# Optimization experiments

Hardware: AMD Instinct MI355X
Metric: run time of the kernel (lower is better)

## Reference

```python
import jax, jax.numpy as jnp
from jax import lax
import numpy as np

HEADS, SAMPLES = 4, 8
B, C, D, H, W = 1, 64, 16, 64, 64
HD = C // HEADS  # head_dim = 16
BN_EPS = 1e-5


def conv3d(x, w, b=None, pad=0):
    out = lax.conv_general_dilated(
        x, w, (1, 1, 1), [(pad, pad)] * 3,
        dimension_numbers=("NCDHW", "OIDHW", "NCDHW"))
    if b is not None:
        out = out + b[None, :, None, None, None]
    return out


def trilinear_sample(vol, grid):
    # vol: [Dv,Hv,Wv,Cc]; grid: [...,3] with torch grid_sample semantics:
    # grid[...,0] -> x (W axis), grid[...,1] -> y (H axis), grid[...,2] -> z (D axis)
    # align_corners=True, padding_mode='border'. Returns [..., Cc].
    Dv, Hv, Wv, _ = vol.shape
    ix = (grid[..., 0] + 1.0) * 0.5 * (Wv - 1)
    iy = (grid[..., 1] + 1.0) * 0.5 * (Hv - 1)
    iz = (grid[..., 2] + 1.0) * 0.5 * (Dv - 1)
    x0 = jnp.floor(ix); y0 = jnp.floor(iy); z0 = jnp.floor(iz)
    wx = (ix - x0)[..., None]; wy = (iy - y0)[..., None]; wz = (iz - z0)[..., None]
    x0i = jnp.clip(x0.astype(jnp.int32), 0, Wv - 1); x1i = jnp.clip(x0i + 1, 0, Wv - 1)
    y0i = jnp.clip(y0.astype(jnp.int32), 0, Hv - 1); y1i = jnp.clip(y0i + 1, 0, Hv - 1)
    z0i = jnp.clip(z0.astype(jnp.int32), 0, Dv - 1); z1i = jnp.clip(z0i + 1, 0, Dv - 1)
    g = lambda z, y, x: vol[z, y, x]
    out = (g(z0i, y0i, x0i) * (1 - wz) * (1 - wy) * (1 - wx)
           + g(z0i, y0i, x1i) * (1 - wz) * (1 - wy) * wx
           + g(z0i, y1i, x0i) * (1 - wz) * wy * (1 - wx)
           + g(z0i, y1i, x1i) * (1 - wz) * wy * wx
           + g(z1i, y0i, x0i) * wz * (1 - wy) * (1 - wx)
           + g(z1i, y0i, x1i) * wz * (1 - wy) * wx
           + g(z1i, y1i, x0i) * wz * wy * (1 - wx)
           + g(z1i, y1i, x1i) * wz * wy * wx)
    return out


def t_deform(feat_prev, feat_curr, p):
    b, c, d, h, w = feat_curr.shape
    kv = conv3d(feat_prev, p["kv_w"], p["kv_b"])          # [B,2C,D,H,W]
    q = conv3d(feat_curr, p["q_w"], p["q_b"])              # [B,C,D,H,W]
    # offset branch: conv3x3 -> GELU(exact) -> conv3x3(no bias) -> tanh
    o = conv3d(feat_curr, p["off1_w"], p["off1_b"], pad=1)
    o = jax.nn.gelu(o, approximate=False)
    o = jnp.tanh(conv3d(o, p["off2_w"], None, pad=1))      # [B,M*S*3,D,H,W]
    off = o.reshape(b, HEADS, SAMPLES, 3, d, h, w).transpose(0, 1, 4, 5, 6, 2, 3)  # [B,M,D,H,W,S,3]
    zz, yy, xx = jnp.meshgrid(jnp.linspace(-1, 1, d), jnp.linspace(-1, 1, h),
                              jnp.linspace(-1, 1, w), indexing="ij")
    base = jnp.stack((zz, yy, xx), axis=-1).astype(feat_curr.dtype)  # [D,H,W,3]
    scale = jnp.array([d, h, w], dtype=feat_curr.dtype)
    grid = base[None, None, :, :, :, None, :] + off / scale
    grid = jnp.clip(grid, -1.0, 1.0)
    grid = grid.transpose(0, 1, 5, 2, 3, 4, 6).reshape(b * HEADS, SAMPLES, d, h, w, 3)
    # channels-last per (batch,head) volume; avoids torch's explicit repeat over samples
    vols = kv.reshape(b, HEADS, 2 * HD, d, h, w).transpose(0, 1, 3, 4, 5, 2)
    vols = vols.reshape(b * HEADS, d, h, w, 2 * HD)
    sampled = jax.vmap(trilinear_sample)(vols, grid)        # [B*M,S,D,H,W,2*HD]
    sampled = sampled.reshape(b, HEADS, SAMPLES, d, h, w, 2 * HD)
    key, value = sampled[..., :HD], sampled[..., HD:]
    qh = q.reshape(b, HEADS, HD, d, h, w) * (HD ** -0.5)
    attn = jnp.einsum("bmcdhw,bmsdhwc->bmsdhw", qh, key)
    attn = jax.nn.softmax(attn, axis=2)
    fused = jnp.einsum("bmsdhw,bmsdhwc->bmcdhw", attn, value).reshape(b, c, d, h, w)
    out = conv3d(fused, p["out_w"], p["out_b"])
    # BatchNorm3d (eval: running stats) + ReLU
    inv = lax.rsqrt(p["bn_var"] + BN_EPS)
    out = (out - p["bn_mean"][None, :, None, None, None]) * (inv * p["bn_gamma"])[None, :, None, None, None] \
          + p["bn_beta"][None, :, None, None, None]
    return jax.nn.relu(out)


def setup_inputs() -> dict:
    key = jax.random.key(0)
    ks = jax.random.split(key, 16)
    r = lambda k, shp, s=0.05: (jax.random.normal(k, shp, dtype=jnp.float32) * s)
    return {
        "mid_feat": jax.random.normal(ks[0], (B, C, D, H, W), dtype=jnp.float32),
        "occ_feat": jax.random.normal(ks[1], (B, C, D, H, W), dtype=jnp.float32),
        "prev_feat": jax.random.normal(ks[2], (B, C, D, H, W), dtype=jnp.float32),
        "off1_w": r(ks[3], (C, C, 3, 3, 3)), "off1_b": r(ks[4], (C,)),
        "off2_w": r(ks[5], (HEADS * SAMPLES * 3, C, 3, 3, 3)),
        "kv_w": r(ks[6], (2 * C, C, 1, 1, 1)), "kv_b": r(ks[7], (2 * C,)),
        "q_w": r(ks[8], (C, C, 1, 1, 1)), "q_b": r(ks[9], (C,)),
        "out_w": r(ks[10], (C, C, 1, 1, 1)), "out_b": r(ks[11], (C,)),
        "bn_gamma": jnp.ones((C,), jnp.float32), "bn_beta": jnp.zeros((C,), jnp.float32),
        "bn_mean": jnp.zeros((C,), jnp.float32), "bn_var": jnp.ones((C,), jnp.float32),
    }


def reference(mid_feat, occ_feat, prev_feat, off1_w, off1_b, off2_w, kv_w, kv_b,
              q_w, q_b, out_w, out_b, bn_gamma, bn_beta, bn_mean, bn_var):
    p = dict(off1_w=off1_w, off1_b=off1_b, off2_w=off2_w, kv_w=kv_w, kv_b=kv_b,
             q_w=q_w, q_b=q_b, out_w=out_w, out_b=out_b, bn_gamma=bn_gamma,
             bn_beta=bn_beta, bn_mean=bn_mean, bn_var=bn_var)
    d1 = t_deform(mid_feat, occ_feat, p)
    d2 = t_deform(mid_feat, prev_feat, p)
    return jnp.concatenate([mid_feat, d1, d2], axis=1)  # [B,3C,D,H,W]
```

## Files before the change

### kernel.cpp

```cpp
#include <hip/hip_runtime.h>
#include <math.h>

#define DD 16
#define HH 64
#define WW 64
#define VV (DD*HH*WW)
#define CC 64
#define NHEADS 4
#define NSAMP 8
#define HDIM 16

typedef unsigned int uint;
typedef unsigned short ushort;
typedef __attribute__((ext_vector_type(8))) short bf16x8;
typedef __attribute__((ext_vector_type(4))) float f32x4;

__device__ __forceinline__ float clampf(float v, float lo, float hi){ return fminf(fmaxf(v, lo), hi); }
__device__ __forceinline__ int imin(int a, int b){ return a < b ? a : b; }

__device__ __forceinline__ ushort f2bf(float f){
  uint u = __float_as_uint(f);
  uint r = (u + 0x7fffu + ((u>>16)&1u)) >> 16;
  return (ushort)r;
}
__device__ __forceinline__ uint packbf2(float a, float b){
  return (uint)f2bf(a) | ((uint)f2bf(b) << 16);
}
__device__ __forceinline__ float bflo(uint u){ return __uint_as_float(u << 16); }
__device__ __forceinline__ float bfhi(uint u){ return __uint_as_float(u & 0xffff0000u); }
__device__ __forceinline__ float bf2f(ushort u){ return __uint_as_float((uint)u << 16); }

__device__ __forceinline__ float fast_tanh(float x){
  float e = __expf(2.f*x);
  return 1.f - 2.f/(e + 1.f);
}

__device__ __forceinline__ bf16x8 make_af(const float* __restrict__ w, int mt, int ks, int lane){
  const float* p = w + (size_t)(mt*16 + (lane&15))*CC + ks*32 + ((lane>>4)<<3);
  float4 f0 = *reinterpret_cast<const float4*>(p);
  float4 f1 = *reinterpret_cast<const float4*>(p+4);
  union { uint4 u; bf16x8 b; } r;
  r.u.x = packbf2(f0.x, f0.y); r.u.y = packbf2(f0.z, f0.w);
  r.u.z = packbf2(f1.x, f1.y); r.u.w = packbf2(f1.z, f1.w);
  return r.b;
}

__device__ __forceinline__ void repack_wmfma_body(const float* __restrict__ w,
                                                  uint* __restrict__ o, int MG, int U){
  int j2 = U & 3;
  int m  = (U>>2) & 15;
  int q  = (U>>6) & 3;
  int rest = U >> 8;
  int g = rest % MG;
  int s = rest / MG;
  int tap = s >> 1, h = s & 1;
  int co = g*16 + m;
  int ci = h*32 + q*8 + j2*2;
  int base = co*1728 + ci*27 + tap;
  o[U] = packbf2(w[base], w[base + 27]);
}
__device__ __forceinline__ void repack_w1_body(const float* __restrict__ w,
                                               uint* __restrict__ o, int MT, int U){
  int j2 = U & 3;
  int lane = (U>>2) & 63;
  int frag = U >> 8;
  int mt = frag % MT;
  int ks = frag / MT;
  int q = lane >> 4, m = lane & 15;
  int co = mt*16 + m;
  int ci = ks*32 + q*8 + j2*2;
  o[U] = packbf2(w[co*CC + ci], w[co*CC + ci + 1]);
}

template<int CO, int EPI>
__device__ void conv1_body(
    int bid, int tid,
    const float* __restrict__ xa, const float* __restrict__ xb,
    const float* __restrict__ wraw, const float* __restrict__ bias,
    void* __restrict__ outp, float* __restrict__ mcopy)
{
  constexpr int MT = CO/16;
  constexpr int MW = MT/4;
  __shared__ ushort xt[64*72];
  int lane = tid & 63;
  int g = __builtin_amdgcn_readfirstlane(tid >> 6);
  int q = lane >> 4, n = lane & 15;
  int call = bid >> 10;
  int v0 = (bid & 1023) * 64;
  bf16x8 afr[2][MW];
  #pragma unroll
  for (int ks=0; ks<2; ks++)
    #pragma unroll
    for (int mw=0; mw<MW; mw++)
      afr[ks][mw] = make_af(wraw, g*MW+mw, ks, lane);
  const float* x = call ? xb : xa;
  for (int it = tid; it < 64*32; it += 256){
    int vox = it & 63; int cp = it >> 6;
    float a = x[(size_t)(2*cp)*VV + v0 + vox];
    float b = x[(size_t)(2*cp+1)*VV + v0 + vox];
    if constexpr (EPI == 0){
      mcopy[(size_t)(2*cp)*VV + v0 + vox] = a;
      mcopy[(size_t)(2*cp+1)*VV + v0 + vox] = b;
    }
    *reinterpret_cast<uint*>(&xt[vox*72 + 2*cp]) = packbf2(a,b);
  }
  __syncthreads();
  f32x4 acc[MW][4];
  #pragma unroll
  for (int mw=0;mw<MW;mw++)
    #pragma unroll
    for (int nt=0;nt<4;nt++){ acc[mw][nt].x=0.f; acc[mw][nt].y=0.f; acc[mw][nt].z=0.f; acc[mw][nt].w=0.f; }
  const char* ldsb = reinterpret_cast<const char*>(xt);
  #pragma unroll
  for (int ks=0; ks<2; ks++){
    bf16x8 bfr[4];
    #pragma unroll
    for (int nt=0; nt<4; nt++)
      bfr[nt] = *reinterpret_cast<const bf16x8*>(ldsb + ((nt*16+n)*144 + q*16 + ks*64));
    #pragma unroll
    for (int mw=0; mw<MW; mw++)
      #pragma unroll
      for (int nt=0; nt<4; nt++)
        acc[mw][nt] = __builtin_amdgcn_mfma_f32_16x16x32_bf16(afr[ks][mw], bfr[nt], acc[mw][nt], 0, 0, 0);
  }
  if constexpr (EPI == 0){
    #pragma unroll
    for (int mw=0; mw<MW; mw++){
      int mt = g*MW + mw;
      int cob = mt*16 + q*4;
      #pragma unroll
      for (int nt=0; nt<4; nt++){
        int v = v0 + nt*16 + n;
        float r0 = acc[mw][nt].x + bias[cob+0];
        float r1 = acc[mw][nt].y + bias[cob+1];
        float r2 = acc[mw][nt].z + bias[cob+2];
        float r3 = acc[mw][nt].w + bias[cob+3];
        int z = v >> 12, y = (v >> 6) & 63, xx = v & 63;
        int head = cob >> 5;
        uint* vols = (uint*)outp;
        uint2 pk; pk.x = packbf2(r0,r1); pk.y = packbf2(r2,r3);
        *reinterpret_cast<uint2*>(vols + ((size_t)head*VV + (size_t)(y*WW+xx)*DD + z)*16 + ((cob&31)>>1)) = pk;
      }
    }
  } else {
    __syncthreads();
    ushort* xr = xt;
    int cob = g*16 + q*4;
    #pragma unroll
    for (int nt=0; nt<4; nt++){
      int vox = nt*16 + n;
      uint2 pk;
      pk.x = packbf2((acc[0][nt].x + bias[cob+0])*0.25f, (acc[0][nt].y + bias[cob+1])*0.25f);
      pk.y = packbf2((acc[0][nt].z + bias[cob+2])*0.25f, (acc[0][nt].w + bias[cob+3])*0.25f);
      *reinterpret_cast<uint2*>(&xr[vox*64 + cob]) = pk;
    }
    __syncthreads();
    char* ob = (char*)((ushort*)outp + (size_t)call*CC*VV) + (size_t)v0*128;
    const char* lb = reinterpret_cast<const char*>(xr);
    #pragma unroll
    for (int k=0; k<2; k++){
      int idx = tid + k*256;
      *reinterpret_cast<uint4*>(ob + idx*16) = *reinterpret_cast<const uint4*>(lb + idx*16);
    }
  }
}

__global__ __launch_bounds__(256) void fused_front(
    const float* __restrict__ occ, const float* __restrict__ prev,
    const float* __restrict__ mid, uint* __restrict__ o0pk,
    const float* __restrict__ off1w, uint* __restrict__ wA1,
    const float* __restrict__ off2w, uint* __restrict__ wA2,
    const float* __restrict__ outw,  uint* __restrict__ wo,
    const float* __restrict__ kvw,  const float* __restrict__ kvb,
    const float* __restrict__ qw,   const float* __restrict__ qb,
    void* __restrict__ vols, void* __restrict__ qbuf, float* __restrict__ out)
{
  int b = blockIdx.x, tid = threadIdx.x;
  if (b < 1024){
    int idx = b*256 + tid;
    int v4 = (idx & (VV/4 - 1)) * 4;
    int rest = idx >> 14;
    int cg = rest & 7;
    int call = rest >> 3;
    const float* x = call ? prev : occ;
    const float* p0 = x + (size_t)(cg*8)*VV + v4;
    float4 f[8];
    #pragma unroll
    for (int c=0;c<8;c++) f[c] = *reinterpret_cast<const float4*>(p0 + (size_t)c*VV);
    uint4* ob = reinterpret_cast<uint4*>(o0pk) + (size_t)(call*8 + cg)*VV + v4;
    #pragma unroll
    for (int j=0;j<4;j++){
      float* fp = reinterpret_cast<float*>(f);
      uint4 w;
      w.x = packbf2(fp[0*4+j], fp[1*4+j]);
      w.y = packbf2(fp[2*4+j], fp[3*4+j]);
      w.z = packbf2(fp[4*4+j], fp[5*4+j]);
      w.w = packbf2(fp[6*4+j], fp[7*4+j]);
      ob[j] = w;
    }
  }
  else if (b < 1240){ repack_wmfma_body(off1w, wA1, 4, (b-1024)*256 + tid); }
  else if (b < 1564){ repack_wmfma_body(off2w, wA2, 6, (b-1240)*256 + tid); }
  else if (b < 1572){ repack_w1_body(outw, wo, 4, (b-1564)*256 + tid); }
  else if (b < 2596){ conv1_body<128,0>(b-1572, tid, mid, nullptr, kvw, kvb, vols, out); }
  else              { conv1_body<64,1>(b-2596, tid, occ, prev, qw, qb, qbuf, nullptr); }
}

template<int CO, int OUTPK, int PREF>
__global__ __launch_bounds__(256) void conv3_mfma(
    const uint* __restrict__ xpk,
    const uint* __restrict__ wA, const float* __restrict__ bias,
    void* __restrict__ outp)
{
  constexpr int MG = CO/16;
  constexpr int MROW = CO/32;
  __shared__ ushort xh[24576];
  int tid = threadIdx.x;
  int lane = tid & 63;
  int w = __builtin_amdgcn_readfirstlane(tid >> 6);
  int q = lane >> 4, n = lane & 15;
  int bid = blockIdx.x;
  int xcd = bid & 7, islot = bid >> 3;
  int call = xcd >> 2;
  int z0 = (xcd & 3) * 4;
  int by = (islot >> 3) << 3, bx = (islot & 7) << 3;

  const uint4* xinp = reinterpret_cast<const uint4*>(xpk) + (size_t)call*8*VV;

  int mbase = (w & 1) * MROW;
  int nzh = (w >> 1) * 2;
  int lo[8];
  #pragma unroll
  for (int nt=0;nt<8;nt++){
    int zi = nzh + (nt>>2);
    int vl = (nt&3)*16 + n;
    lo[nt] = (zi*100 + (vl>>3)*10 + (vl&7))*80 + q*16;
  }
  f32x4 acc[MROW][8];
  #pragma unroll
  for (int mr=0;mr<MROW;mr++)
    #pragma unroll
    for (int nt=0;nt<8;nt++){ acc[mr][nt].x=0.f; acc[mr][nt].y=0.f; acc[mr][nt].z=0.f; acc[mr][nt].w=0.f; }

  const char* ldsb = reinterpret_cast<const char*>(xh);
  const char* wac  = reinterpret_cast<const char*>(wA);

  auto compute_half = [&](int h){
    #pragma unroll 2
    for (int tap=0; tap<27; tap++){
      int dz = tap/9; int r9 = tap - dz*9; int dy = r9/3; int dxx = r9 - dy*3;
      int stepOff = (dz*100 + dy*10 + dxx)*80;
      int s = tap*2 + h;
      bf16x8 af[MROW];
      #pragma unroll
      for (int mr=0;mr<MROW;mr++)
        af[mr] = *reinterpret_cast<const bf16x8*>(wac + (size_t)((s*MG + mbase+mr)*64 + lane)*16);
      bf16x8 bf[8];
      #pragma unroll
      for (int nt=0;nt<8;nt++)
        bf[nt] = *reinterpret_cast<const bf16x8*>(ldsb + (lo[nt] + stepOff));
      #pragma unroll
      for (int mr=0;mr<MROW;mr++)
        #pragma unroll
        for (int nt=0;nt<8;nt++)
          acc[mr][nt] = __builtin_amdgcn_mfma_f32_16x16x32_bf16(af[mr], bf[nt], acc[mr][nt], 0, 0, 0);
    }
  };

  if constexpr (PREF){
    uint4 pq[10];
    auto load_half = [&](int h){
      #pragma unroll
      for (int k=0;k<10;k++){
        int it = tid + k*256;
        if (it < 2400){
          int cg = it/600; int pos = it - cg*600;
          int dz = pos/100; int rr = pos - dz*100; int dy = rr/10; int dxx = rr - dy*10;
          int gz = z0 + dz - 1, gy = by + dy - 1, gx = bx + dxx - 1;
          uint4 v; v.x = 0u; v.y = 0u; v.z = 0u; v.w = 0u;
          if (gz>=0 && gz<DD && gy>=0 && gy<HH && gx>=0 && gx<WW)
            v = xinp[(size_t)(h*4+cg)*VV + (size_t)((gz*HH+gy)*WW + gx)];
          pq[k] = v;
        }
      }
    };
    auto write_half = [&](){
      #pragma unroll
      for (int k=0;k<10;k++){
        int it = tid + k*256;
        if (it < 2400){
          int cg = it/600; int pos = it - cg*600;
          *reinterpret_cast<uint4*>(&xh[pos*40 + cg*8]) = pq[k];
        }
      }
    };
    load_half(0);
    write_half();
    __syncthreads();
    load_half(1);
    compute_half(0);
    __syncthreads();
    write_half();
    __syncthreads();
    compute_half(1);
  } else {
    #pragma unroll 1
    for (int h=0; h<2; h++){
      if (h) __syncthreads();
      for (int k=0;k<10;k++){
        int it = tid + k*256;
        if (it < 2400){
          int cg = it/600; int pos = it - cg*600;
          int dz = pos/100; int rr = pos - dz*100; int dy = rr/10; int dxx = rr - dy*10;
          int gz = z0 + dz - 1, gy = by + dy - 1, gx = bx + dxx - 1;
          uint4 v; v.x = 0u; v.y = 0u; v.z = 0u; v.w = 0u;
          if (gz>=0 && gz<DD && gy>=0 && gy<HH && gx>=0 && gx<WW)
            v = xinp[(size_t)(h*4+cg)*VV + (size_t)((gz*HH+gy)*WW + gx)];
          *reinterpret_cast<uint4*>(&xh[pos*40 + cg*8]) = v;
        }
      }
      __syncthreads();
      compute_half(h);
    }
  }

  if (OUTPK == 1){
    #pragma unroll
    for (int mr=0; mr<MROW; mr++){
      int cob = (mbase+mr)*16 + q*4;
      #pragma unroll
      for (int nt=0; nt<8; nt++){
        int zi = nzh + (nt>>2);
        int vl = (nt&3)*16 + n;
        int vy = by + (vl>>3), vx = bx + (vl&7);
        size_t gv = (size_t)(((z0+zi)*HH + vy)*WW + vx);
        float r0 = acc[mr][nt].x + bias[cob+0];
        float r1 = acc[mr][nt].y + bias[cob+1];
        float r2 = acc[mr][nt].z + bias[cob+2];
        float r3 = acc[mr][nt].w + bias[cob+3];
        r0 = 0.5f*r0*(1.f + erff(r0*0.70710678118654752f));
        r1 = 0.5f*r1*(1.f + erff(r1*0.70710678118654752f));
        r2 = 0.5f*r2*(1.f + erff(r2*0.70710678118654752f));
        r3 = 0.5f*r3*(1.f + erff(r3*0.70710678118654752f));
        uint2 pk; pk.x = packbf2(r0,r1); pk.y = packbf2(r2,r3);
        uint* dst = (uint*)outp;
        *reinterpret_cast<uint2*>(dst + ((size_t)(call*8 + (cob>>3))*VV + gv)*4 + ((cob&4)>>1)) = pk;
      }
    }
  } else {
    __syncthreads();
    ushort* xr = xh;
    #pragma unroll
    for (int mr=0; mr<MROW; mr++){
      int cob = (mbase+mr)*16 + q*4;
      #pragma unroll
      for (int nt=0; nt<8; nt++){
        int row = (nzh + (nt>>2))*64 + (nt&3)*16 + n;
        uint2 pk;
        pk.x = packbf2(fast_tanh(acc[mr][nt].x), fast_tanh(acc[mr][nt].y));
        pk.y = packbf2(fast_tanh(acc[mr][nt].z), fast_tanh(acc[mr][nt].w));
        *reinterpret_cast<uint2*>(&xr[row*96 + cob]) = pk;
      }
    }
    __syncthreads();
    ushort* dst = (ushort*)outp + (size_t)call*96*VV;
    const char* lb = reinterpret_cast<const char*>(xr);
    #pragma unroll
    for (int k=0; k<12; k++){
      int idx = tid + k*256;
      int chunk = idx/96;
      int off = idx - chunk*96;
      int zi = chunk>>3, y8 = chunk&7;
      size_t gb = (size_t)(((z0+zi)*HH + by + y8)*WW + bx)*192 + (size_t)off*16;
      *reinterpret_cast<uint4*>((char*)dst + gb) = *reinterpret_cast<const uint4*>(lb + idx*16);
    }
  }
}

struct Geom { int x0,x1,y0,y1,z0,z1; float wx,wy,wz; };
__device__ __forceinline__ Geom make_geom(float zb, float yb, float xb,
                                          float o0, float o1, float o2){
  float g0 = clampf(zb + o0*(1.f/16.f), -1.f, 1.f);
  float g1 = clampf(yb + o1*(1.f/64.f), -1.f, 1.f);
  float g2 = clampf(xb + o2*(1.f/64.f), -1.f, 1.f);
  float ix = (g0+1.f)*0.5f*63.f;
  float iy = (g1+1.f)*0.5f*63.f;
  float iz = (g2+1.f)*0.5f*15.f;
  float fx=floorf(ix), fy=floorf(iy), fz=floorf(iz);
  Geom g;
  g.wx = ix-fx; g.wy = iy-fy; g.wz = iz-fz;
  g.x0 = (int)fx; g.x1 = imin(g.x0+1, WW-1);
  g.y0 = (int)fy; g.y1 = imin(g.y0+1, HH-1);
  g.z0 = (int)fz; g.z1 = imin(g.z0+1, DD-1);
  return g;
}

__global__ __launch_bounds__(256) void sample_attn_kernel(
    const ushort* __restrict__ qbuf, const ushort* __restrict__ offbuf,
    const uint* __restrict__ vols, const uint* __restrict__ woA,
    const float* __restrict__ outb, const float* __restrict__ bng,
    const float* __restrict__ bnb, const float* __restrict__ bnm,
    const float* __restrict__ bnv, float* __restrict__ dout)
{
  __shared__ ushort fsb[16*72];
  int t = threadIdx.x;
  int lane = t & 63;
  int m = __builtin_amdgcn_readfirstlane(t >> 6);
  int slot = lane >> 2;
  int r = lane & 3;
  int bid = blockIdx.x;
  int xcd = bid & 7, islot = bid >> 3;
  int call = islot >> 9;
  int z = xcd*2 + ((islot >> 8) & 1);
  int rem = islot & 255;
  int y = rem >> 2;
  int x0 = (rem & 3) << 4;
  int x = x0 + slot;
  int vbase = (z*HH + y)*WW + x0;
  int v = vbase + slot;

  const ushort* qb = qbuf   + (size_t)call*CC*VV;
  const ushort* ob = offbuf + (size_t)call*96*VV;

  uint4 qu = *reinterpret_cast<const uint4*>(qb + (size_t)v*64 + m*16 + (r&1)*8);
  float qf[8];
  qf[0]=bflo(qu.x); qf[1]=bfhi(qu.x); qf[2]=bflo(qu.y); qf[3]=bfhi(qu.y);
  qf[4]=bflo(qu.z); qf[5]=bfhi(qu.z); qf[6]=bflo(qu.w); qf[7]=bfhi(qu.w);

  uint ou[12];
  {
    const uint4* op4 = reinterpret_cast<const uint4*>(ob + (size_t)v*96 + m*24);
    uint4 a = op4[0], b4 = op4[1], c4 = op4[2];
    ou[0]=a.x;  ou[1]=a.y;  ou[2]=a.z;  ou[3]=a.w;
    ou[4]=b4.x; ou[5]=b4.y; ou[6]=b4.z; ou[7]=b4.w;
    ou[8]=c4.x; ou[9]=c4.y; ou[10]=c4.z; ou[11]=c4.w;
  }

  float zbf = -1.f + (float)z*(2.f/15.f);
  float ybf = -1.f + (float)y*(2.f/63.f);
  float xbf = -1.f + (float)x*(2.f/63.f);

  const char* volb = reinterpret_cast<const char*>(vols) + (size_t)m*VV*64;
  float roleK = (r < 2) ? 1.f : 0.f;
  float lrun = 0.f;
  float fused[8];
  #pragma unroll
  for (int c=0;c<8;c++) fused[c]=0.f;

  #pragma unroll
  for (int s=0;s<NSAMP;s++){
    int i0 = 3*s, i1 = 3*s+1, i2 = 3*s+2;
    float o0 = (i0&1) ? bfhi(ou[i0>>1]) : bflo(ou[i0>>1]);
    float o1 = (i1&1) ? bfhi(ou[i1>>1]) : bflo(ou[i1>>1]);
    float o2 = (i2&1) ? bfhi(ou[i2>>1]) : bflo(ou[i2>>1]);
    Geom g = make_geom(zbf,ybf,xbf,o0,o1,o2);
    int tz0 = g.z0*64 + r*16;
    int tz1 = g.z1*64 + r*16;
    float wx1 = g.wx, wx0 = 1.f-g.wx;
    float wy1 = g.wy, wy0 = 1.f-g.wy;
    float wz1 = g.wz, wz0 = 1.f-g.wz;
    float acc[8];
    #pragma unroll
    for (int c=0;c<8;c++) acc[c]=0.f;
    #pragma unroll
    for (int ky=0;ky<2;ky++)
    #pragma unroll
    for (int kx=0;kx<2;kx++){
      int cy = ky? g.y1:g.y0, cx = kx? g.x1:g.x0;
      float wyx = (ky? wy1:wy0)*(kx? wx1:wx0);
      float a0 = wyx*wz0, a1 = wyx*wz1;
      uint wzp;
      asm("v_cvt_pk_bf16_f32 %0, %1, %2" : "=v"(wzp) : "v"(a0), "v"(a1));
      int tb = ((cy<<6) + cx) << 10;
      const char* p = volb + tb;
      uint4 u0 = *reinterpret_cast<const uint4*>(p + tz0);
      uint4 u1 = *reinterpret_cast<const uint4*>(p + tz1);
      uint plo, phi;
      plo = __builtin_amdgcn_perm(u1.x, u0.x, 0x05040100u);
      phi = __builtin_amdgcn_perm(u1.x, u0.x, 0x07060302u);
      asm("v_dot2_f32_bf16 %0, %1, %2, %0" : "+v"(acc[0]) : "v"(plo), "v"(wzp));
      asm("v_dot2_f32_bf16 %0, %1, %2, %0" : "+v"(acc[1]) : "v"(phi), "v"(wzp));
      plo = __builtin_amdgcn_perm(u1.y, u0.y, 0x05040100u);
      phi = __builtin_amdgcn_perm(u1.y, u0.y, 0x07060302u);
      asm("v_dot2_f32_bf16 %0, %1, %2, %0" : "+v"(acc[2]) : "v"(plo), "v"(wzp));
      asm("v_dot2_f32_bf16 %0, %1, %2, %0" : "+v"(acc[3]) : "v"(phi), "v"(wzp));
      plo = __builtin_amdgcn_perm(u1.z, u0.z, 0x05040100u);
      phi = __builtin_amdgcn_perm(u1.z, u0.z, 0x07060302u);
      asm("v_dot2_f32_bf16 %0, %1, %2, %0" : "+v"(acc[4]) : "v"(plo), "v"(wzp));
      asm("v_dot2_f32_bf16 %0, %1, %2, %0" : "+v"(acc[5]) : "v"(phi), "v"(wzp));
      plo = __builtin_amdgcn_perm(u1.w, u0.w, 0x05040100u);
      phi = __builtin_amdgcn_perm(u1.w, u0.w, 0x07060302u);
      asm("v_dot2_f32_bf16 %0, %1, %2, %0" : "+v"(acc[6]) : "v"(plo), "v"(wzp));
      asm("v_dot2_f32_bf16 %0, %1, %2, %0" : "+v"(acc[7]) : "v"(phi), "v"(wzp));
    }
    float h = qf[0]*acc[0]+qf[1]*acc[1]+qf[2]*acc[2]+qf[3]*acc[3]
            + qf[4]*acc[4]+qf[5]*acc[5]+qf[6]*acc[6]+qf[7]*acc[7];
    h *= roleK;
    h += __shfl_xor(h, 1);
    h += __shfl_xor(h, 2);
    float e = __expf(h);
    lrun += e;
    #pragma unroll
    for (int c=0;c<8;c++) fused[c] += e*acc[c];
  }
  float isum = 1.f/lrun;
  if (r >= 2){
    uint4 pk;
    pk.x = packbf2(fused[0]*isum, fused[1]*isum);
    pk.y = packbf2(fused[2]*isum, fused[3]*isum);
    pk.z = packbf2(fused[4]*isum, fused[5]*isum);
    pk.w = packbf2(fused[6]*isum, fused[7]*isum);
    *reinterpret_cast<uint4*>(&fsb[slot*72 + m*16 + (r&1)*8]) = pk;
  }
  __syncthreads();

  int qq = lane >> 4, n = lane & 15;
  f32x4 acco;
  acco.x=0.f; acco.y=0.f; acco.z=0.f; acco.w=0.f;
  const char* ldsb = reinterpret_cast<const char*>(fsb);
  const char* wac  = reinterpret_cast<const char*>(woA);
  #pragma unroll
  for (int ks=0; ks<2; ks++){
    bf16x8 af = *reinterpret_cast<const bf16x8*>(wac + (size_t)((ks*4 + m)*64 + lane)*16);
    bf16x8 bfv = *reinterpret_cast<const bf16x8*>(ldsb + (n*144 + qq*16 + ks*64));
    acco = __builtin_amdgcn_mfma_f32_16x16x32_bf16(af, bfv, acco, 0, 0, 0);
  }
  int choff = 64 + call*64;
  #pragma unroll
  for (int rr=0; rr<4; rr++){
    int co = m*16 + qq*4 + rr;
    float inv = rsqrtf(bnv[co] + 1e-5f) * bng[co];
    float val = (acco[rr] + outb[co] - bnm[co]) * inv + bnb[co];
    val = fmaxf(val, 0.f);
    dout[(size_t)(choff+co)*VV + vbase + n] = val;
  }
}

extern "C" void kernel_launch(void* const* d_in, const int* in_sizes, int n_in,
                              void* d_out, int out_size, void* d_ws, size_t ws_size,
                              hipStream_t stream){
  (void)in_sizes; (void)n_in; (void)out_size; (void)ws_size;
  const float* mid  = (const float*)d_in[0];
  const float* occ  = (const float*)d_in[1];
  const float* prev = (const float*)d_in[2];
  const float* off1w= (const float*)d_in[3];
  const float* off1b= (const float*)d_in[4];
  const float* off2w= (const float*)d_in[5];
  const float* kvw  = (const float*)d_in[6];
  const float* kvb  = (const float*)d_in[7];
  const float* qw   = (const float*)d_in[8];
  const float* qb   = (const float*)d_in[9];
  const float* outw = (const float*)d_in[10];
  const float* outb = (const float*)d_in[11];
  const float* bng  = (const float*)d_in[12];
  const float* bnb  = (const float*)d_in[13];
  const float* bnm  = (const float*)d_in[14];
  const float* bnv  = (const float*)d_in[15];
  float* out = (float*)d_out;

  uint*   vols  = (uint*)d_ws;
  ushort* qbuf  = (ushort*)(vols + (size_t)4*VV*16);
  uint*   o1pk  = (uint*)(qbuf + (size_t)2*CC*VV);
  ushort* offb  = (ushort*)(o1pk + (size_t)2*32*VV);
  uint*   wA1   = (uint*)(offb + (size_t)2*96*VV);
  uint*   wA2   = wA1 + 55296;
  uint*   wo    = wA2 + 82944;
  uint*   o0pk  = wo  + 2048;

  fused_front<<<4644, 256, 0, stream>>>(occ, prev, mid, o0pk,
      off1w, wA1, off2w, wA2, outw, wo, kvw, kvb, qw, qb,
      (void*)vols, (void*)qbuf, out);
  conv3_mfma<64,1,1><<<512, 256, 0, stream>>>(o0pk, wA1, off1b, (void*)o1pk);
  conv3_mfma<96,0,0><<<512, 256, 0, stream>>>(o1pk, wA2, off1b, (void*)offb);
  sample_attn_kernel<<<8192, 256, 0, stream>>>(qbuf, offb, vols, wo,
      outb, bng, bnb, bnm, bnv, out);
}
```

Baseline: 311.8 us.

## Move q 1x1 conv into conv3a kernel reading packed bf16 input

The q projection is taken out of the front kernel and launched as extra blocks in the first 3x3 offset conv kernel. It now reads the already-packed bf16 o0pk buffer with uint4 loads instead of re-reading and converting the fp32 inputs. The front kernel shrinks, conv3a gains independent blocks that can fill idle CUs alongside the 512 conv blocks, and the second conv now uses the prefetch variant. The trade-off is that the conv1 blocks share the larger 48KB LDS allocation, which may limit their occupancy.

```diff
diff --git a/kernel.cpp b/kernel.cpp
--- a/kernel.cpp
+++ b/kernel.cpp
@@ -74,14 +74,13 @@
 
 template<int CO, int EPI>
 __device__ void conv1_body(
-    int bid, int tid,
-    const float* __restrict__ xa, const float* __restrict__ xb,
+    int bid, int tid, ushort* __restrict__ xt,
+    const float* __restrict__ xf, const uint* __restrict__ xq,
     const float* __restrict__ wraw, const float* __restrict__ bias,
     void* __restrict__ outp, float* __restrict__ mcopy)
 {
   constexpr int MT = CO/16;
   constexpr int MW = MT/4;
-  __shared__ ushort xt[64*72];
   int lane = tid & 63;
   int g = __builtin_amdgcn_readfirstlane(tid >> 6);
   int q = lane >> 4, n = lane & 15;
@@ -93,16 +92,21 @@
     #pragma unroll
     for (int mw=0; mw<MW; mw++)
       afr[ks][mw] = make_af(wraw, g*MW+mw, ks, lane);
-  const float* x = call ? xb : xa;
-  for (int it = tid; it < 64*32; it += 256){
-    int vox = it & 63; int cp = it >> 6;
-    float a = x[(size_t)(2*cp)*VV + v0 + vox];
-    float b = x[(size_t)(2*cp+1)*VV + v0 + vox];
-    if constexpr (EPI == 0){
+  if constexpr (EPI == 0){
+    for (int it = tid; it < 64*32; it += 256){
+      int vox = it & 63; int cp = it >> 6;
+      float a = xf[(size_t)(2*cp)*VV + v0 + vox];
+      float b = xf[(size_t)(2*cp+1)*VV + v0 + vox];
       mcopy[(size_t)(2*cp)*VV + v0 + vox] = a;
       mcopy[(size_t)(2*cp+1)*VV + v0 + vox] = b;
-    }
-    *reinterpret_cast<uint*>(&xt[vox*72 + 2*cp]) = packbf2(a,b);
+      *reinterpret_cast<uint*>(&xt[vox*72 + 2*cp]) = packbf2(a,b);
+    }
+  } else {
+    const uint4* xp = reinterpret_cast<const uint4*>(xq) + (size_t)call*8*VV;
+    for (int it = tid; it < 64*8; it += 256){
+      int vox = it & 63; int cg = it >> 6;
+      *reinterpret_cast<uint4*>(&xt[vox*72 + cg*8]) = xp[(size_t)cg*VV + v0 + vox];
+    }
   }
   __syncthreads();
   f32x4 acc[MW][4];
@@ -165,61 +169,18 @@
   }
 }
 
-__global__ __launch_bounds__(256) void fused_front(
-    const float* __restrict__ occ, const float* __restrict__ prev,
-    const float* __restrict__ mid, uint* __restrict__ o0pk,
-    const float* __restrict__ off1w, uint* __restrict__ wA1,
-    const float* __restrict__ off2w, uint* __restrict__ wA2,
-    const float* __restrict__ outw,  uint* __restrict__ wo,
-    const float* __restrict__ kvw,  const float* __restrict__ kvb,
-    const float* __restrict__ qw,   const float* __restrict__ qb,
-    void* __restrict__ vols, void* __restrict__ qbuf, float* __restrict__ out)
-{
-  int b = blockIdx.x, tid = threadIdx.x;
-  if (b < 1024){
-    int idx = b*256 + tid;
-    int v4 = (idx & (VV/4 - 1)) * 4;
-    int rest = idx >> 14;
-    int cg = rest & 7;
-    int call = rest >> 3;
-    const float* x = call ? prev : occ;
-    const float* p0 = x + (size_t)(cg*8)*VV + v4;
-    float4 f[8];
-    #pragma unroll
-    for (int c=0;c<8;c++) f[c] = *reinterpret_cast<const float4*>(p0 + (size_t)c*VV);
-    uint4* ob = reinterpret_cast<uint4*>(o0pk) + (size_t)(call*8 + cg)*VV + v4;
-    #pragma unroll
-    for (int j=0;j<4;j++){
-      float* fp = reinterpret_cast<float*>(f);
-      uint4 w;
-      w.x = packbf2(fp[0*4+j], fp[1*4+j]);
-      w.y = packbf2(fp[2*4+j], fp[3*4+j]);
-      w.z = packbf2(fp[4*4+j], fp[5*4+j]);
-      w.w = packbf2(fp[6*4+j], fp[7*4+j]);
-      ob[j] = w;
-    }
-  }
-  else if (b < 1240){ repack_wmfma_body(off1w, wA1, 4, (b-1024)*256 + tid); }
-  else if (b < 1564){ repack_wmfma_body(off2w, wA2, 6, (b-1240)*256 + tid); }
-  else if (b < 1572){ repack_w1_body(outw, wo, 4, (b-1564)*256 + tid); }
-  else if (b < 2596){ conv1_body<128,0>(b-1572, tid, mid, nullptr, kvw, kvb, vols, out); }
-  else              { conv1_body<64,1>(b-2596, tid, occ, prev, qw, qb, qbuf, nullptr); }
-}
-
 template<int CO, int OUTPK, int PREF>
-__global__ __launch_bounds__(256) void conv3_mfma(
+__device__ void conv3_body(
+    int bid, int tid, ushort* __restrict__ xh,
     const uint* __restrict__ xpk,
     const uint* __restrict__ wA, const float* __restrict__ bias,
     void* __restrict__ outp)
 {
   constexpr int MG = CO/16;
   constexpr int MROW = CO/32;
-  __shared__ ushort xh[24576];
-  int tid = threadIdx.x;
   int lane = tid & 63;
   int w = __builtin_amdgcn_readfirstlane(tid >> 6);
   int q = lane >> 4, n = lane & 15;
-  int bid = blockIdx.x;
   int xcd = bid & 7, islot = bid >> 3;
   int call = xcd >> 2;
   int z0 = (xcd & 3) * 4;
@@ -375,6 +336,66 @@
       *reinterpret_cast<uint4*>((char*)dst + gb) = *reinterpret_cast<const uint4*>(lb + idx*16);
     }
   }
+}
+
+__global__ __launch_bounds__(256) void fused_front(
+    const float* __restrict__ occ, const float* __restrict__ prev,
+    const float* __restrict__ mid, uint* __restrict__ o0pk,
+    const float* __restrict__ off1w, uint* __restrict__ wA1,
+    const float* __restrict__ off2w, uint* __restrict__ wA2,
+    const float* __restrict__ outw,  uint* __restrict__ wo,
+    const float* __restrict__ kvw,  const float* __restrict__ kvb,
+    void* __restrict__ vols, float* __restrict__ out)
+{
+  __shared__ ushort lds[64*72];
+  int b = blockIdx.x, tid = threadIdx.x;
+  if (b < 1024){
+    int idx = b*256 + tid;
+    int v4 = (idx & (VV/4 - 1)) * 4;
+    int rest = idx >> 14;
+    int cg = rest & 7;
+    int call = rest >> 3;
+    const float* x = call ? prev : occ;
+    const float* p0 = x + (size_t)(cg*8)*VV + v4;
+    float4 f[8];
+    #pragma unroll
+    for (int c=0;c<8;c++) f[c] = *reinterpret_cast<const float4*>(p0 + (size_t)c*VV);
+    uint4* ob = reinterpret_cast<uint4*>(o0pk) + (size_t)(call*8 + cg)*VV + v4;
+    #pragma unroll
+    for (int j=0;j<4;j++){
+      float* fp = reinterpret_cast<float*>(f);
+      uint4 w;
+      w.x = packbf2(fp[0*4+j], fp[1*4+j]);
+      w.y = packbf2(fp[2*4+j], fp[3*4+j]);
+      w.z = packbf2(fp[4*4+j], fp[5*4+j]);
+      w.w = packbf2(fp[6*4+j], fp[7*4+j]);
+      ob[j] = w;
+    }
+  }
+  else if (b < 1240){ repack_wmfma_body(off1w, wA1, 4, (b-1024)*256 + tid); }
+  else if (b < 1564){ repack_wmfma_body(off2w, wA2, 6, (b-1240)*256 + tid); }
+  else if (b < 1572){ repack_w1_body(outw, wo, 4, (b-1564)*256 + tid); }
+  else              { conv1_body<128,0>(b-1572, tid, lds, mid, nullptr, kvw, kvb, vols, out); }
+}
+
+__global__ __launch_bounds__(256) void conv3a_q(
+    const uint* __restrict__ o0pk, const uint* __restrict__ wA1,
+    const float* __restrict__ off1b, void* __restrict__ o1pk,
+    const float* __restrict__ qw, const float* __restrict__ qb,
+    void* __restrict__ qbuf)
+{
+  __shared__ ushort lds[24576];
+  int b = blockIdx.x, tid = threadIdx.x;
+  if (b < 512) conv3_body<64,1,1>(b, tid, lds, o0pk, wA1, off1b, o1pk);
+  else         conv1_body<64,1>(b-512, tid, lds, nullptr, o0pk, qw, qb, qbuf, nullptr);
+}
+
+__global__ __launch_bounds__(256) void conv3b(
+    const uint* __restrict__ o1pk, const uint* __restrict__ wA2,
+    const float* __restrict__ off1b, void* __restrict__ offb)
+{
+  __shared__ ushort lds[24576];
+  conv3_body<96,0,1>(blockIdx.x, threadIdx.x, lds, o1pk, wA2, off1b, offb);
 }
 
 struct Geom { int x0,x1,y0,y1,z0,z1; float wx,wy,wz; };
@@ -567,11 +588,12 @@
   uint*   wo    = wA2 + 82944;
   uint*   o0pk  = wo  + 2048;
 
-  fused_front<<<4644, 256, 0, stream>>>(occ, prev, mid, o0pk,
-      off1w, wA1, off2w, wA2, outw, wo, kvw, kvb, qw, qb,
-      (void*)vols, (void*)qbuf, out);
-  conv3_mfma<64,1,1><<<512, 256, 0, stream>>>(o0pk, wA1, off1b, (void*)o1pk);
-  conv3_mfma<96,0,0><<<512, 256, 0, stream>>>(o1pk, wA2, off1b, (void*)offb);
+  fused_front<<<2596, 256, 0, stream>>>(occ, prev, mid, o0pk,
+      off1w, wA1, off2w, wA2, outw, wo, kvw, kvb,
+      (void*)vols, out);
+  conv3a_q<<<2560, 256, 0, stream>>>(o0pk, wA1, off1b, (void*)o1pk,
+      qw, qb, (void*)qbuf);
+  conv3b<<<512, 256, 0, stream>>>(o1pk, wA2, off1b, (void*)offb);
   sample_attn_kernel<<<8192, 256, 0, stream>>>(qbuf, offb, vols, wo,
       outb, bng, bnb, bnm, bnv, out);
 }
```

Result: slower. 327.9 us (+5.2%).
